# Kernel tuning notes

Hardware: AMD Instinct MI355X
Metric: run time of the kernel (lower is better)

The kernel has to match this reference:

```python
import jax, jax.numpy as jnp
import numpy as np
import math

B, T, E, F, K, NUM_CONV, H = 32, 2048, 512, 512, 7, 4, 8
EPS = 1e-5


def _ln2(x):
    # fresh nn.LayerNorm(x.size()[1:]): normalize jointly over last two dims, weight=1 bias=0
    mu = jnp.mean(x, axis=(-2, -1), keepdims=True)
    var = jnp.var(x, axis=(-2, -1), keepdims=True)
    return (x - mu) * jax.lax.rsqrt(var + EPS)


def _ds_conv(x, dw_w, dw_b, pw_w, pw_b):
    # x: (B, C, T); depthwise conv (groups=C) then pointwise 1x1
    C = x.shape[1]
    k = dw_w.shape[-1]
    y = jax.lax.conv_general_dilated(
        x, dw_w, window_strides=(1,), padding=[(k // 2, k // 2)],
        dimension_numbers=('NCH', 'OIH', 'NCH'), feature_group_count=C)
    y = y + dw_b[None, :, None]
    y = jnp.einsum('oc,bct->bot', pw_w, y) + pw_b[None, :, None]
    return y


def _pos_enc(n, e):
    # pe[i, 0::2] = sin(i * div), pe[i, 1::2] = cos(i * div); returns (n, 1, e)
    pos = jnp.arange(n, dtype=jnp.float32)[:, None]
    div = jnp.exp(jnp.arange(0, e, 2, dtype=jnp.float32) * (-math.log(10000.0) / e))
    pe = jnp.zeros((n, e), dtype=jnp.float32)
    pe = pe.at[:, 0::2].set(jnp.sin(pos * div)).at[:, 1::2].set(jnp.cos(pos * div))
    return pe[:, None, :]


def setup_inputs() -> dict:
    key = jax.random.key(0)
    ks = jax.random.split(key, 20)
    w = lambda i, shape: (jax.random.normal(ks[i], shape, jnp.float32) * 0.02)
    return {
        'x': jax.random.normal(ks[0], (B, T, E), jnp.float32),
        'dw1_w': w(1, (E, 1, K)), 'dw1_b': w(2, (E,)),
        'pw1_w': w(3, (F, E)), 'pw1_b': w(4, (F,)),
        'dw2_w': w(5, (F, 1, K)), 'dw2_b': w(6, (F,)),
        'pw2_w': w(7, (F, F)), 'pw2_b': w(8, (F,)),
        'wq': w(9, (F, F)), 'bq': w(10, (F,)),
        'wk': w(11, (F, F)), 'bk': w(12, (F,)),
        'wv': w(13, (F, F)), 'bv': w(14, (F,)),
        'wp': w(15, (F, F)), 'bp': w(16, (F,)),
        'ff_w': w(17, (F, F)), 'ff_b': w(18, (F,)),
    }


def reference(x, dw1_w, dw1_b, pw1_w, pw1_b, dw2_w, dw2_b, pw2_w, pw2_b,
              wq, bq, wk, bk, wv, bv, wp, bp, ff_w, ff_b):
    b, t, e = x.shape
    # positional encoding: pe[:x.size(0)] -> (B,1,E), broadcast over T (faithful quirk)
    x = x + _pos_enc(b, e)
    x = jnp.transpose(x, (0, 2, 1))          # (B, E, T)
    x = _ln2(x)
    x = _ds_conv(x, dw1_w, dw1_b, pw1_w, pw1_b)   # (B, F, T)
    for _ in range(NUM_CONV - 1):                 # shared conv weights each iter (faithful)
        x = x + _ds_conv(_ln2(x), dw2_w, dw2_b, pw2_w, pw2_b)
    # attention: code permutes to (T, B, F) so attention attends across the batch axis
    y = jnp.transpose(_ln2(x), (2, 0, 1))    # (T, B, F)
    x = jnp.transpose(x, (2, 0, 1))          # (T, B, F)
    f = x.shape[-1]
    hd = f // H
    q = (y @ wq.T + bq).reshape(t, b, H, hd).transpose(0, 2, 1, 3)  # (T, H, B, hd)
    k = (y @ wk.T + bk).reshape(t, b, H, hd).transpose(0, 2, 1, 3)
    v = (y @ wv.T + bv).reshape(t, b, H, hd).transpose(0, 2, 1, 3)
    att = jnp.einsum('thbd,thcd->thbc', q, k) * (1.0 / math.sqrt(hd))
    att = jax.nn.softmax(att, axis=-1)
    yo = jnp.einsum('thbc,thcd->thbd', att, v)
    yo = yo.transpose(0, 2, 1, 3).reshape(t, b, f)
    yo = yo @ wp.T + bp
    x = x + yo
    y = _ln2(x)                               # norm over last-two dims (B, F)
    y = y @ ff_w.T + ff_b
    x = x + y
    return jnp.transpose(x, (1, 0, 2))        # (B, T, F)
```

## Files before the change

### kernel.cpp

```cpp
#include <hip/hip_runtime.h>
#include <math.h>

constexpr int B_ = 32, T_ = 2048, E_ = 512, F_ = 512, KW = 7, H_ = 8;
constexpr float EPS_ = 1e-5f;

typedef unsigned short bfu;
typedef __attribute__((ext_vector_type(8))) unsigned short ushort8v;
typedef __attribute__((ext_vector_type(8))) short short8v;
typedef __attribute__((ext_vector_type(4))) short short4v;
typedef __attribute__((ext_vector_type(4))) float f32x4;
typedef __attribute__((ext_vector_type(16))) float f32x16;
typedef const __attribute__((address_space(1))) void* gp1_t;
typedef __attribute__((address_space(3))) void* lp3_t;

__device__ __forceinline__ float b2f(bfu u) {
    return __uint_as_float(((unsigned)u) << 16);
}
__device__ __forceinline__ bfu f2b(float f) {
    unsigned i = __float_as_uint(f);
    i += 0x7fffu + ((i >> 16) & 1u);
    return (bfu)(i >> 16);
}

template <typename T> __device__ __forceinline__ void stv(T* p, size_t i, float v);
template <> __device__ __forceinline__ void stv<bfu>(bfu* p, size_t i, float v)   { p[i] = f2b(v); }
template <> __device__ __forceinline__ void stv<float>(float* p, size_t i, float v) { p[i] = v; }

__global__ void zero_kernel(float* p, int n) {
    int i = blockIdx.x * 256 + threadIdx.x;
    if (i < n) p[i] = 0.f;
}

__global__ __launch_bounds__(256) void prep(const float* __restrict__ w0, const float* __restrict__ w1,
                                            const float* __restrict__ w2, const float* __restrict__ w3,
                                            const float* __restrict__ w4, const float* __restrict__ w5,
                                            const float* __restrict__ w6,
                                            bfu* __restrict__ wb, float* __restrict__ pe) {
    int idx = blockIdx.x * 256 + threadIdx.x;
    if (idx < 7 * 65536) {
        int w = idx >> 16, off = (idx & 65535) * 4;
        const float* src = w0;
        switch (w) {
            case 1: src = w1; break; case 2: src = w2; break; case 3: src = w3; break;
            case 4: src = w4; break; case 5: src = w5; break; case 6: src = w6; break;
            default: break;
        }
        float4 v = *(const float4*)(src + off);
        ushort4 u = { f2b(v.x), f2b(v.y), f2b(v.z), f2b(v.w) };
        *(ushort4*)(wb + (size_t)w * 262144 + off) = u;
    } else {
        int i = (idx - 7 * 65536) * 4;
        if (i < 16384) {
            #pragma unroll
            for (int e4 = 0; e4 < 4; e4++) {
                int ii = i + e4;
                int b = ii >> 9, e = ii & 511;
                float div = expf(-(float)(e & ~1) * (logf(10000.0f) / (float)E_));
                float ang = (float)b * div;
                pe[ii] = (e & 1) ? cosf(ang) : sinf(ang);
            }
        }
    }
}

__global__ __launch_bounds__(256) void add_pe(const float* __restrict__ x,
                                              const float* __restrict__ pe,
                                              bfu* __restrict__ out,
                                              float* __restrict__ stats) {
    size_t base = (size_t)blockIdx.x * 4096;
    int b = (int)(base >> 20);
    float sum = 0.f, sq = 0.f;
    #pragma unroll
    for (int u = 0; u < 4; u++) {
        size_t i = base + u * 1024 + threadIdx.x * 4;
        int e = (int)(i & 511);
        float4 xv = *(const float4*)(x + i);
        float4 pv = *(const float4*)(pe + (b << 9) + e);
        float a0 = xv.x + pv.x, a1 = xv.y + pv.y, a2 = xv.z + pv.z, a3 = xv.w + pv.w;
        ushort4 o = { f2b(a0), f2b(a1), f2b(a2), f2b(a3) };
        *(ushort4*)(out + i) = o;
        sum += a0 + a1 + a2 + a3;
        sq  += a0 * a0 + a1 * a1 + a2 * a2 + a3 * a3;
    }
    #pragma unroll
    for (int off = 32; off > 0; off >>= 1) {
        sum += __shfl_down(sum, off, 64);
        sq  += __shfl_down(sq,  off, 64);
    }
    __shared__ float ss[8];
    int lane = threadIdx.x & 63, wv = threadIdx.x >> 6;
    if (lane == 0) { ss[wv] = sum; ss[4 + wv] = sq; }
    __syncthreads();
    if (threadIdx.x == 0) {
        atomicAdd(&stats[2 * b],     ss[0] + ss[1] + ss[2] + ss[3]);
        atomicAdd(&stats[2 * b + 1], ss[4] + ss[5] + ss[6] + ss[7]);
    }
}

__device__ __forceinline__ float ln_rstd(float sumsq, float mu, float invL) {
    float var = fmaxf(sumsq * invL - mu * mu, 0.f);
    return rsqrtf(var + EPS_);
}

__global__ __launch_bounds__(256) void dwconv_nhwc(const bfu* __restrict__ x,
                                                   const float* __restrict__ stats,
                                                   const float* __restrict__ w,
                                                   const float* __restrict__ bias,
                                                   bfu* __restrict__ out) {
    __shared__ float ws[64 * 57];
    int tid = threadIdx.x;
    int b = blockIdx.z;
    for (int i = tid; i < F_ * KW; i += 256) {
        int f = i / KW, dt = i - f * KW;
        ws[(f >> 3) * 57 + (f & 7) * 7 + dt] = w[i];
    }
    __syncthreads();
    const float invL = 1.0f / (float)(F_ * T_);
    float mu   = stats[2 * b] * invL;
    float rstd = ln_rstd(stats[2 * b + 1], mu, invL);
    int f0 = (tid & 63) * 8;
    int t  = blockIdx.x * 4 + (tid >> 6);
    const bfu* xb = x + (size_t)b * T_ * F_;
    const float* wc_ = &ws[(tid & 63) * 57];
    float acc[8];
    #pragma unroll
    for (int j = 0; j < 8; j++) acc[j] = bias[f0 + j];
    #pragma unroll
    for (int dt = 0; dt < KW; dt++) {
        int tt = t + dt - KW / 2;
        if (tt >= 0 && tt < T_) {
            ushort8v v = *(const ushort8v*)(xb + (size_t)tt * F_ + f0);
            #pragma unroll
            for (int j = 0; j < 8; j++)
                acc[j] += wc_[j * 7 + dt] * ((b2f(v[j]) - mu) * rstd);
        }
    }
    ushort8v o;
    #pragma unroll
    for (int j = 0; j < 8; j++) o[j] = f2b(acc[j]);
    *(ushort8v*)(out + ((size_t)b * T_ + t) * F_ + f0) = o;
}

template <typename OutT, int GMODE>
__global__ __launch_bounds__(256) void gemm_mfma(const bfu* __restrict__ A,
                                                 const bfu* __restrict__ Wb,
                                                 const float* __restrict__ bias,
                                                 const bfu* res, OutT* out,
                                                 int out_transpose, float* stats) {
    constexpr int Kd = 512;
    __shared__ bfu As[128 * 32];
    __shared__ bfu Bs[128 * 32];
    int id  = blockIdx.x;
    int swz = (id & 7) * 256 + (id >> 3);
    int m0 = (swz & 3) * 128;
    int r0 = (swz >> 2) * 128;
    int tid  = threadIdx.x;
    int wave = tid >> 6, lane = tid & 63;
    int wr = (wave >> 1) * 64, wc = (wave & 1) * 64;
    int lg = lane >> 4,  lr = lane & 15;

    const char* Ab = (const char*)A  + (size_t)r0 * 1024;
    const char* Bb = (const char*)Wb + (size_t)m0 * 1024;
    char* AsB = (char*)As;
    char* BsB = (char*)Bs;
    int rS = (wave << 4) + (lane >> 2);
    int kb = (lane & 3) << 4;
    int ldsoff = wave << 10;

    f32x4 acc[4][4];
    #pragma unroll
    for (int mi = 0; mi < 4; mi++)
        #pragma unroll
        for (int ni = 0; ni < 4; ni++)
            acc[mi][ni] = (f32x4){0.f, 0.f, 0.f, 0.f};

    const bfu* ApL = As + (wr + lr) * 32 + lg * 8;
    const bfu* BpL = Bs + (wc + lr) * 32 + lg * 8;

    for (int k0 = 0; k0 < Kd; k0 += 32) {
        size_t koff = (size_t)(k0 << 1);
        const char* a0 = Ab + (size_t)rS * 1024 + koff + kb;
        const char* b0 = Bb + (size_t)rS * 1024 + koff + kb;
        __builtin_amdgcn_global_load_lds((gp1_t)a0,           (lp3_t)(AsB + ldsoff),        16, 0, 0);
        __builtin_amdgcn_global_load_lds((gp1_t)(a0 + 65536), (lp3_t)(AsB + ldsoff + 4096), 16, 0, 0);
        __builtin_amdgcn_global_load_lds((gp1_t)b0,           (lp3_t)(BsB + ldsoff),        16, 0, 0);
        __builtin_amdgcn_global_load_lds((gp1_t)(b0 + 65536), (lp3_t)(BsB + ldsoff + 4096), 16, 0, 0);
        __syncthreads();
        short8v a[4], bb[4];
        #pragma unroll
        for (int mi = 0; mi < 4; mi++) a[mi]  = *(const short8v*)(ApL + mi * 512);
        #pragma unroll
        for (int ni = 0; ni < 4; ni++) bb[ni] = *(const short8v*)(BpL + ni * 512);
        #pragma unroll
        for (int mi = 0; mi < 4; mi++)
            #pragma unroll
            for (int ni = 0; ni < 4; ni++)
                acc[mi][ni] = __builtin_amdgcn_mfma_f32_16x16x32_bf16(a[mi], bb[ni], acc[mi][ni], 0, 0, 0);
        __syncthreads();
    }

    float sAcc0 = 0.f, sAcc1 = 0.f, qAcc0 = 0.f, qAcc1 = 0.f;
    #pragma unroll
    for (int ni = 0; ni < 4; ni++) {
        int m = m0 + wc + ni * 16 + lr;
        float bv = bias[m];
        #pragma unroll
        for (int mi = 0; mi < 4; mi++) {
            #pragma unroll
            for (int j = 0; j < 4; j++) {
                int r = r0 + wr + mi * 16 + lg * 4 + j;
                float v = acc[mi][ni][j] + bv;
                if (res) v += b2f(res[(size_t)r * 512 + m]);
                if (GMODE) {
                    if (mi < 2) { sAcc0 += v; qAcc0 += v * v; }
                    else        { sAcc1 += v; qAcc1 += v * v; }
                }
                if (!out_transpose) {
                    stv(out, (size_t)r * 512 + m, v);
                } else {
                    int t = r >> 5, bb2 = r & 31;
                    stv(out, ((size_t)bb2 * T_ + t) * 512 + m, v);
                }
            }
        }
    }
    if (GMODE == 1) {
        float s = sAcc0 + sAcc1, q = qAcc0 + qAcc1;
        #pragma unroll
        for (int off = 32; off > 0; off >>= 1) {
            s += __shfl_down(s, off, 64);
            q += __shfl_down(q, off, 64);
        }
        if (lane == 0) {
            int g = r0 >> 11;
            atomicAdd(&stats[2 * g], s);
            atomicAdd(&stats[2 * g + 1], q);
        }
    } else if (GMODE == 2) {
        #pragma unroll
        for (int off = 32; off > 0; off >>= 1) {
            sAcc0 += __shfl_down(sAcc0, off, 64); qAcc0 += __shfl_down(qAcc0, off, 64);
            sAcc1 += __shfl_down(sAcc1, off, 64); qAcc1 += __shfl_down(qAcc1, off, 64);
        }
        if (lane == 0) {
            int g0 = (r0 >> 5) + (wr >> 5);
            atomicAdd(&stats[2 * g0],     sAcc0);
            atomicAdd(&stats[2 * g0 + 1], qAcc0);
            atomicAdd(&stats[2 * g0 + 2], sAcc1);
            atomicAdd(&stats[2 * g0 + 3], qAcc1);
        }
    }
}

__global__ __launch_bounds__(256) void bt2tb_ln(const bfu* __restrict__ x,
                                                const float* __restrict__ stats,
                                                bfu* __restrict__ xa,
                                                bfu* __restrict__ yln) {
    size_t i = ((size_t)blockIdx.x * 256 + threadIdx.x) * 8;
    int f = (int)(i & 511);
    size_t bt = i >> 9;
    int t = (int)(bt & 2047);
    int b = (int)(bt >> 11);
    const float invL = 1.0f / (float)(F_ * T_);
    float mu   = stats[2 * b] * invL;
    float rstd = ln_rstd(stats[2 * b + 1], mu, invL);
    ushort8v v = *(const ushort8v*)(x + i);
    size_t dst = (((size_t)t * B_ + b) << 9) + f;
    *(ushort8v*)(xa + dst) = v;
    ushort8v o;
    #pragma unroll
    for (int j = 0; j < 8; j++) o[j] = f2b((b2f(v[j]) - mu) * rstd);
    *(ushort8v*)(yln + dst) = o;
}

__global__ __launch_bounds__(256) void ln_apply(const bfu* __restrict__ x,
                                                const float* __restrict__ stats,
                                                bfu* __restrict__ out,
                                                float invL, int shift) {
    size_t i = ((size_t)blockIdx.x * 256 + threadIdx.x) * 8;
    int g = (int)(i >> shift);
    float mu   = stats[2 * g] * invL;
    float rstd = ln_rstd(stats[2 * g + 1], mu, invL);
    ushort8v v = *(const ushort8v*)(x + i);
    ushort8v o;
    #pragma unroll
    for (int j = 0; j < 8; j++) o[j] = f2b((b2f(v[j]) - mu) * rstd);
    *(ushort8v*)(out + i) = o;
}

__global__ __launch_bounds__(256) void attention_mfma(const bfu* __restrict__ Q,
                                                      const bfu* __restrict__ K,
                                                      const bfu* __restrict__ V,
                                                      bfu* __restrict__ O) {
    __shared__ bfu vt[4][64 * 36];
    int tid = threadIdx.x;
    int wave = tid >> 6, lane = tid & 63;
    int wid = blockIdx.x * 4 + wave;
    int t = wid >> 3, h = wid & 7;
    int lh = lane >> 5, lm = lane & 31;
    size_t base = (size_t)t * (B_ * F_) + (size_t)h * 64;

    short8v qf[4], kf[4];
    const bfu* qrow = Q + base + (size_t)lm * F_ + lh * 8;
    const bfu* krow = K + base + (size_t)lm * F_ + lh * 8;
    #pragma unroll
    for (int s = 0; s < 4; s++) {
        qf[s] = *(const short8v*)(qrow + s * 16);
        kf[s] = *(const short8v*)(krow + s * 16);
    }
    bfu* vt_w = vt[wave];
    {
        int c = lane >> 1, d0 = (lane & 1) * 32;
        const bfu* vrow = V + base + (size_t)c * F_ + d0;
        #pragma unroll
        for (int j = 0; j < 4; j++) {
            ushort8v vv = *(const ushort8v*)(vrow + j * 8);
            #pragma unroll
            for (int e = 0; e < 8; e++)
                vt_w[(d0 + j * 8 + e) * 36 + c] = vv[e];
        }
    }
    f32x16 st;
    #pragma unroll
    for (int r = 0; r < 16; r++) st[r] = 0.f;
    #pragma unroll
    for (int s = 0; s < 4; s++)
        st = __builtin_amdgcn_mfma_f32_32x32x16_bf16(kf[s], qf[s], st, 0, 0, 0);

    float p[16];
    float mx = -1e30f;
    #pragma unroll
    for (int r = 0; r < 16; r++) { p[r] = st[r] * 0.125f; mx = fmaxf(mx, p[r]); }
    mx = fmaxf(mx, __shfl_xor(mx, 32, 64));
    float sum = 0.f;
    #pragma unroll
    for (int r = 0; r < 16; r++) { p[r] = expf(p[r] - mx); sum += p[r]; }
    sum += __shfl_xor(sum, 32, 64);
    float inv = 1.0f / sum;
    short8v pa[2];
    #pragma unroll
    for (int j = 0; j < 8; j++) {
        pa[0][j] = (short)f2b(p[j] * inv);
        pa[1][j] = (short)f2b(p[8 + j] * inv);
    }
    f32x16 oacc[2];
    #pragma unroll
    for (int dt = 0; dt < 2; dt++)
        #pragma unroll
        for (int r = 0; r < 16; r++) oacc[dt][r] = 0.f;
    #pragma unroll
    for (int dt = 0; dt < 2; dt++) {
        const bfu* vr = vt_w + (dt * 32 + lm) * 36 + lh * 4;
        #pragma unroll
        for (int kh = 0; kh < 2; kh++) {
            short4v b0 = *(const short4v*)(vr + kh * 16);
            short4v b1 = *(const short4v*)(vr + kh * 16 + 8);
            short8v bf;
            #pragma unroll
            for (int e = 0; e < 4; e++) { bf[e] = b0[e]; bf[4 + e] = b1[e]; }
            oacc[dt] = __builtin_amdgcn_mfma_f32_32x32x16_bf16(pa[kh], bf, oacc[dt], 0, 0, 0);
        }
    }
    bfu* orow = O + base + lm;
    #pragma unroll
    for (int dt = 0; dt < 2; dt++)
        #pragma unroll
        for (int r = 0; r < 16; r++) {
            int b = (r & 3) + 8 * (r >> 2) + 4 * lh;
            orow[(size_t)b * F_ + dt * 32] = f2b(oacc[dt][r]);
        }
}

extern "C" void kernel_launch(void* const* d_in, const int* in_sizes, int n_in,
                              void* d_out, int out_size, void* d_ws, size_t ws_size,
                              hipStream_t stream) {
    const float* x     = (const float*)d_in[0];
    const float* dw1_w = (const float*)d_in[1];
    const float* dw1_b = (const float*)d_in[2];
    const float* pw1_w = (const float*)d_in[3];
    const float* pw1_b = (const float*)d_in[4];
    const float* dw2_w = (const float*)d_in[5];
    const float* dw2_b = (const float*)d_in[6];
    const float* pw2_w = (const float*)d_in[7];
    const float* pw2_b = (const float*)d_in[8];
    const float* wq = (const float*)d_in[9];   const float* bq = (const float*)d_in[10];
    const float* wk = (const float*)d_in[11];  const float* bk = (const float*)d_in[12];
    const float* wv = (const float*)d_in[13];  const float* bv = (const float*)d_in[14];
    const float* wp = (const float*)d_in[15];  const float* bp = (const float*)d_in[16];
    const float* ffw = (const float*)d_in[17]; const float* ffb = (const float*)d_in[18];
    float* out = (float*)d_out;

    const size_t SZ = (size_t)B_ * F_ * T_;
    const size_t WN = (size_t)F_ * F_;

    float* stats = (float*)d_ws;
    float* stA = stats;
    float* st1 = stats + 128;
    float* st2 = stats + 256;
    float* st3 = stats + 384;
    float* st4 = stats + 512;
    float* stT = stats + 1024;
    float* peTab = stats + 8192;
    bfu*   wBuf  = (bfu*)(peTab + 16384);
    bfu* wb_pw1 = wBuf + 0 * WN;
    bfu* wb_pw2 = wBuf + 1 * WN;
    bfu* wb_q   = wBuf + 2 * WN;
    bfu* wb_k   = wBuf + 3 * WN;
    bfu* wb_v   = wBuf + 4 * WN;
    bfu* wb_p   = wBuf + 5 * WN;
    bfu* wb_ff  = wBuf + 6 * WN;
    bfu* bufX = (bfu*)d_ws + (1 << 21);
    bfu* bufC = bufX + SZ;
    bfu* bufY = bufC + SZ;
    bfu* bufK = bufY + SZ;
    bfu* bufV = bufK + SZ;

    zero_kernel<<<32, 256, 0, stream>>>(stats, 8192);
    prep<<<1808, 256, 0, stream>>>(pw1_w, pw2_w, wq, wk, wv, wp, ffw, wBuf, peTab);
    add_pe<<<8192, 256, 0, stream>>>(x, peTab, bufX, stA);

    dwconv_nhwc<<<dim3(T_ / 4, 1, B_), 256, 0, stream>>>(bufX, stA, dw1_w, dw1_b, bufC);
    gemm_mfma<bfu, 1><<<2048, 256, 0, stream>>>(bufC, wb_pw1, pw1_b, nullptr, bufX, 0, st1);

    float* sts[3] = { st2, st3, st4 };
    for (int it = 0; it < 3; ++it) {
        float* sin_ = (it == 0) ? st1 : sts[it - 1];
        dwconv_nhwc<<<dim3(T_ / 4, 1, B_), 256, 0, stream>>>(bufX, sin_, dw2_w, dw2_b, bufC);
        gemm_mfma<bfu, 1><<<2048, 256, 0, stream>>>(bufC, wb_pw2, pw2_b, bufX, bufX, 0, sts[it]);
    }

    bt2tb_ln<<<16384, 256, 0, stream>>>(bufX, st4, bufC, bufY);

    gemm_mfma<bfu, 0><<<2048, 256, 0, stream>>>(bufY, wb_q, bq, nullptr, bufX, 0, nullptr);
    gemm_mfma<bfu, 0><<<2048, 256, 0, stream>>>(bufY, wb_k, bk, nullptr, bufK, 0, nullptr);
    gemm_mfma<bfu, 0><<<2048, 256, 0, stream>>>(bufY, wb_v, bv, nullptr, bufV, 0, nullptr);

    attention_mfma<<<4096, 256, 0, stream>>>(bufX, bufK, bufV, bufY);

    gemm_mfma<bfu, 2><<<2048, 256, 0, stream>>>(bufY, wb_p, bp, bufC, bufK, 0, stT);

    ln_apply<<<16384, 256, 0, stream>>>(bufK, stT, bufX, 1.0f / (float)(B_ * F_), 14);

    gemm_mfma<float, 0><<<2048, 256, 0, stream>>>(bufX, wb_ff, ffb, bufK, out, 1, nullptr);
}
```

Measured before the change: 1.825 ms.

## Double-buffer GEMM LDS loads, fuse QKV GEMMs, vectorize epilogue stores

The MFMA GEMM now double-buffers its LDS tiles, issuing the next k-slice's global_load_lds before computing the current one, with explicit vmcnt waits and raw s_barrier in place of two __syncthreads per iteration. The Q, K and V projections are merged into one launch of 6144 workgroups that picks the weight, bias and output by tile index. The MFMA operands are swapped so each lane holds four consecutive output columns, which lets the epilogue use float4 bias loads and 4-wide vector stores and residual loads. The aim is to hide load latency, cut launch count and reduce scattered scalar stores, at the cost of doubled LDS and a launch_bounds occupancy hint.

```diff
diff --git a/kernel.cpp b/kernel.cpp
--- a/kernel.cpp
+++ b/kernel.cpp
@@ -22,9 +22,15 @@
     return (bfu)(i >> 16);
 }
 
-template <typename T> __device__ __forceinline__ void stv(T* p, size_t i, float v);
-template <> __device__ __forceinline__ void stv<bfu>(bfu* p, size_t i, float v)   { p[i] = f2b(v); }
-template <> __device__ __forceinline__ void stv<float>(float* p, size_t i, float v) { p[i] = v; }
+template <typename T> __device__ __forceinline__ void st4(T* p, size_t i, float a, float b, float c, float d);
+template <> __device__ __forceinline__ void st4<bfu>(bfu* p, size_t i, float a, float b, float c, float d) {
+    ushort4 u = { f2b(a), f2b(b), f2b(c), f2b(d) };
+    *(ushort4*)(p + i) = u;
+}
+template <> __device__ __forceinline__ void st4<float>(float* p, size_t i, float a, float b, float c, float d) {
+    float4 u = { a, b, c, d };
+    *(float4*)(p + i) = u;
+}
 
 __global__ void zero_kernel(float* p, int n) {
     int i = blockIdx.x * 256 + threadIdx.x;
@@ -141,86 +147,117 @@
     *(ushort8v*)(out + ((size_t)b * T_ + t) * F_ + f0) = o;
 }
 
-template <typename OutT, int GMODE>
-__global__ __launch_bounds__(256) void gemm_mfma(const bfu* __restrict__ A,
-                                                 const bfu* __restrict__ Wb,
-                                                 const float* __restrict__ bias,
-                                                 const bfu* res, OutT* out,
-                                                 int out_transpose, float* stats) {
+template <typename OutT, int GMODE, int NMAT>
+__global__ __launch_bounds__(256, 4) void gemm_mfma(const bfu* __restrict__ A,
+                                                    const bfu* __restrict__ Wb,
+                                                    const float* __restrict__ bias0,
+                                                    const float* __restrict__ bias1,
+                                                    const float* __restrict__ bias2,
+                                                    const bfu* res,
+                                                    OutT* out0, OutT* out1, OutT* out2,
+                                                    int out_transpose, float* stats) {
     constexpr int Kd = 512;
-    __shared__ bfu As[128 * 32];
-    __shared__ bfu Bs[128 * 32];
+    constexpr int NWG = 2048 * NMAT;
+    __shared__ bfu As[2][4096];
+    __shared__ bfu Bs[2][4096];
     int id  = blockIdx.x;
-    int swz = (id & 7) * 256 + (id >> 3);
-    int m0 = (swz & 3) * 128;
-    int r0 = (swz >> 2) * 128;
+    int swz = (id & 7) * (NWG >> 3) + (id >> 3);
+    int mt  = swz % (4 * NMAT);
+    int r0  = (swz / (4 * NMAT)) * 128;
+    int mat = mt >> 2;
+    int m0  = (mt & 3) * 128;
     int tid  = threadIdx.x;
     int wave = tid >> 6, lane = tid & 63;
     int wr = (wave >> 1) * 64, wc = (wave & 1) * 64;
     int lg = lane >> 4,  lr = lane & 15;
 
     const char* Ab = (const char*)A  + (size_t)r0 * 1024;
-    const char* Bb = (const char*)Wb + (size_t)m0 * 1024;
-    char* AsB = (char*)As;
-    char* BsB = (char*)Bs;
+    const char* Bb = (const char*)Wb + (size_t)mt * 128 * 1024;
     int rS = (wave << 4) + (lane >> 2);
     int kb = (lane & 3) << 4;
     int ldsoff = wave << 10;
 
     f32x4 acc[4][4];
     #pragma unroll
-    for (int mi = 0; mi < 4; mi++)
+    for (int ni = 0; ni < 4; ni++)
+        #pragma unroll
+        for (int mi = 0; mi < 4; mi++)
+            acc[ni][mi] = (f32x4){0.f, 0.f, 0.f, 0.f};
+
+    #define STAGE(p, k0)                                                                   \
+        do {                                                                               \
+            size_t koff_ = (size_t)((k0) << 1);                                            \
+            const char* a0_ = Ab + (size_t)rS * 1024 + koff_ + kb;                         \
+            const char* b0_ = Bb + (size_t)rS * 1024 + koff_ + kb;                         \
+            char* ad_ = (char*)As + (p) * 8192 + ldsoff;                                   \
+            char* bd_ = (char*)Bs + (p) * 8192 + ldsoff;                                   \
+            __builtin_amdgcn_global_load_lds((gp1_t)a0_,           (lp3_t)ad_,          16, 0, 0); \
+            __builtin_amdgcn_global_load_lds((gp1_t)(a0_ + 65536), (lp3_t)(ad_ + 4096), 16, 0, 0); \
+            __builtin_amdgcn_global_load_lds((gp1_t)b0_,           (lp3_t)bd_,          16, 0, 0); \
+            __builtin_amdgcn_global_load_lds((gp1_t)(b0_ + 65536), (lp3_t)(bd_ + 4096), 16, 0, 0); \
+        } while (0)
+
+    STAGE(0, 0);
+    #pragma unroll 2
+    for (int it = 0; it < 16; ++it) {
+        int cur = it & 1;
+        if (it < 15) {
+            STAGE(cur ^ 1, (it + 1) * 32);
+            asm volatile("s_waitcnt vmcnt(4)" ::: "memory");
+        } else {
+            asm volatile("s_waitcnt vmcnt(0)" ::: "memory");
+        }
+        __builtin_amdgcn_sched_barrier(0);
+        __builtin_amdgcn_s_barrier();
+        __builtin_amdgcn_sched_barrier(0);
+        const bfu* Ap = &As[cur][(wr + lr) * 32 + lg * 8];
+        const bfu* Bp = &Bs[cur][(wc + lr) * 32 + lg * 8];
+        short8v a[4], bb[4];
+        #pragma unroll
+        for (int mi = 0; mi < 4; mi++) a[mi]  = *(const short8v*)(Ap + mi * 512);
+        #pragma unroll
+        for (int ni = 0; ni < 4; ni++) bb[ni] = *(const short8v*)(Bp + ni * 512);
         #pragma unroll
         for (int ni = 0; ni < 4; ni++)
-            acc[mi][ni] = (f32x4){0.f, 0.f, 0.f, 0.f};
-
-    const bfu* ApL = As + (wr + lr) * 32 + lg * 8;
-    const bfu* BpL = Bs + (wc + lr) * 32 + lg * 8;
-
-    for (int k0 = 0; k0 < Kd; k0 += 32) {
-        size_t koff = (size_t)(k0 << 1);
-        const char* a0 = Ab + (size_t)rS * 1024 + koff + kb;
-        const char* b0 = Bb + (size_t)rS * 1024 + koff + kb;
-        __builtin_amdgcn_global_load_lds((gp1_t)a0,           (lp3_t)(AsB + ldsoff),        16, 0, 0);
-        __builtin_amdgcn_global_load_lds((gp1_t)(a0 + 65536), (lp3_t)(AsB + ldsoff + 4096), 16, 0, 0);
-        __builtin_amdgcn_global_load_lds((gp1_t)b0,           (lp3_t)(BsB + ldsoff),        16, 0, 0);
-        __builtin_amdgcn_global_load_lds((gp1_t)(b0 + 65536), (lp3_t)(BsB + ldsoff + 4096), 16, 0, 0);
-        __syncthreads();
-        short8v a[4], bb[4];
-        #pragma unroll
-        for (int mi = 0; mi < 4; mi++) a[mi]  = *(const short8v*)(ApL + mi * 512);
-        #pragma unroll
-        for (int ni = 0; ni < 4; ni++) bb[ni] = *(const short8v*)(BpL + ni * 512);
-        #pragma unroll
-        for (int mi = 0; mi < 4; mi++)
             #pragma unroll
-            for (int ni = 0; ni < 4; ni++)
-                acc[mi][ni] = __builtin_amdgcn_mfma_f32_16x16x32_bf16(a[mi], bb[ni], acc[mi][ni], 0, 0, 0);
-        __syncthreads();
-    }
+            for (int mi = 0; mi < 4; mi++)
+                acc[ni][mi] = __builtin_amdgcn_mfma_f32_16x16x32_bf16(bb[ni], a[mi], acc[ni][mi], 0, 0, 0);
+        asm volatile("s_waitcnt lgkmcnt(0)" ::: "memory");
+        __builtin_amdgcn_sched_barrier(0);
+        __builtin_amdgcn_s_barrier();
+    }
+    #undef STAGE
+
+    const float* bias = (NMAT == 1 || mat == 0) ? bias0 : (mat == 1 ? bias1 : bias2);
+    OutT*        outb = (NMAT == 1 || mat == 0) ? out0  : (mat == 1 ? out1  : out2);
 
     float sAcc0 = 0.f, sAcc1 = 0.f, qAcc0 = 0.f, qAcc1 = 0.f;
     #pragma unroll
-    for (int ni = 0; ni < 4; ni++) {
-        int m = m0 + wc + ni * 16 + lr;
-        float bv = bias[m];
-        #pragma unroll
-        for (int mi = 0; mi < 4; mi++) {
-            #pragma unroll
-            for (int j = 0; j < 4; j++) {
-                int r = r0 + wr + mi * 16 + lg * 4 + j;
-                float v = acc[mi][ni][j] + bv;
-                if (res) v += b2f(res[(size_t)r * 512 + m]);
-                if (GMODE) {
-                    if (mi < 2) { sAcc0 += v; qAcc0 += v * v; }
-                    else        { sAcc1 += v; qAcc1 += v * v; }
-                }
-                if (!out_transpose) {
-                    stv(out, (size_t)r * 512 + m, v);
-                } else {
-                    int t = r >> 5, bb2 = r & 31;
-                    stv(out, ((size_t)bb2 * T_ + t) * 512 + m, v);
-                }
+    for (int mi = 0; mi < 4; mi++) {
+        int r = r0 + wr + mi * 16 + lr;
+        #pragma unroll
+        for (int ni = 0; ni < 4; ni++) {
+            int mo = m0 + wc + ni * 16 + lg * 4;
+            float4 bv = *(const float4*)(bias + mo);
+            float v0 = acc[ni][mi][0] + bv.x;
+            float v1 = acc[ni][mi][1] + bv.y;
+            float v2 = acc[ni][mi][2] + bv.z;
+            float v3 = acc[ni][mi][3] + bv.w;
+            if (res) {
+                ushort4 rv = *(const ushort4*)(res + (size_t)r * 512 + mo);
+                v0 += b2f(rv.x); v1 += b2f(rv.y); v2 += b2f(rv.z); v3 += b2f(rv.w);
+            }
+            if (GMODE) {
+                float s = v0 + v1 + v2 + v3;
+                float q = v0 * v0 + v1 * v1 + v2 * v2 + v3 * v3;
+                if (mi < 2) { sAcc0 += s; qAcc0 += q; }
+                else        { sAcc1 += s; qAcc1 += q; }
+            }
+            if (!out_transpose) {
+                st4(outb, (size_t)r * 512 + mo, v0, v1, v2, v3);
+            } else {
+                int t = r >> 5, bb2 = r & 31;
+                st4(outb, ((size_t)bb2 * T_ + t) * 512 + mo, v0, v1, v2, v3);
             }
         }
     }
@@ -405,8 +442,6 @@
     bfu* wb_pw1 = wBuf + 0 * WN;
     bfu* wb_pw2 = wBuf + 1 * WN;
     bfu* wb_q   = wBuf + 2 * WN;
-    bfu* wb_k   = wBuf + 3 * WN;
-    bfu* wb_v   = wBuf + 4 * WN;
     bfu* wb_p   = wBuf + 5 * WN;
     bfu* wb_ff  = wBuf + 6 * WN;
     bfu* bufX = (bfu*)d_ws + (1 << 21);
@@ -420,26 +455,29 @@
     add_pe<<<8192, 256, 0, stream>>>(x, peTab, bufX, stA);
 
     dwconv_nhwc<<<dim3(T_ / 4, 1, B_), 256, 0, stream>>>(bufX, stA, dw1_w, dw1_b, bufC);
-    gemm_mfma<bfu, 1><<<2048, 256, 0, stream>>>(bufC, wb_pw1, pw1_b, nullptr, bufX, 0, st1);
+    gemm_mfma<bfu, 1, 1><<<2048, 256, 0, stream>>>(bufC, wb_pw1, pw1_b, pw1_b, pw1_b,
+                                                   nullptr, bufX, bufX, bufX, 0, st1);
 
     float* sts[3] = { st2, st3, st4 };
     for (int it = 0; it < 3; ++it) {
         float* sin_ = (it == 0) ? st1 : sts[it - 1];
         dwconv_nhwc<<<dim3(T_ / 4, 1, B_), 256, 0, stream>>>(bufX, sin_, dw2_w, dw2_b, bufC);
-        gemm_mfma<bfu, 1><<<2048, 256, 0, stream>>>(bufC, wb_pw2, pw2_b, bufX, bufX, 0, sts[it]);
+        gemm_mfma<bfu, 1, 1><<<2048, 256, 0, stream>>>(bufC, wb_pw2, pw2_b, pw2_b, pw2_b,
+                                                       bufX, bufX, bufX, bufX, 0, sts[it]);
     }
 
     bt2tb_ln<<<16384, 256, 0, stream>>>(bufX, st4, bufC, bufY);
 
-    gemm_mfma<bfu, 0><<<2048, 256, 0, stream>>>(bufY, wb_q, bq, nullptr, bufX, 0, nullptr);
-    gemm_mfma<bfu, 0><<<2048, 256, 0, stream>>>(bufY, wb_k, bk, nullptr, bufK, 0, nullptr);
-    gemm_mfma<bfu, 0><<<2048, 256, 0, stream>>>(bufY, wb_v, bv, nullptr, bufV, 0, nullptr);
+    gemm_mfma<bfu, 0, 3><<<6144, 256, 0, stream>>>(bufY, wb_q, bq, bk, bv,
+                                                   nullptr, bufX, bufK, bufV, 0, nullptr);
 
     attention_mfma<<<4096, 256, 0, stream>>>(bufX, bufK, bufV, bufY);
 
-    gemm_mfma<bfu, 2><<<2048, 256, 0, stream>>>(bufY, wb_p, bp, bufC, bufK, 0, stT);
+    gemm_mfma<bfu, 2, 1><<<2048, 256, 0, stream>>>(bufY, wb_p, bp, bp, bp,
+                                                   bufC, bufK, bufK, bufK, 0, stT);
 
     ln_apply<<<16384, 256, 0, stream>>>(bufK, stT, bufX, 1.0f / (float)(B_ * F_), 14);
 
-    gemm_mfma<float, 0><<<2048, 256, 0, stream>>>(bufX, wb_ff, ffb, bufK, out, 1, nullptr);
-}
+    gemm_mfma<float, 0, 1><<<2048, 256, 0, stream>>>(bufX, wb_ff, ffb, ffb, ffb,
+                                                     bufK, out, out, out, 1, nullptr);
+}
```

After: 1.600 ms. 1.14x faster.
